# Kernel tuning notes

Measured on AMD Instinct MI355X. Metric: run time of the kernel, lower is better.

The kernel has to match this reference:

```python
import jax, jax.numpy as jnp
from jax import lax
import numpy as np

B, T, D, H, L, O = 64, 256, 256, 256, 50, 2


def setup_inputs() -> dict:
    key = jax.random.key(0)
    ks = jax.random.split(key, 7)
    s = 0.05  # small init to keep gates out of saturation
    return {
        "x": jax.random.normal(ks[0], (B, T, D), jnp.float32),
        "W_ih": jax.random.normal(ks[1], (L, 4 * H, H), jnp.float32) * s,
        "W_hh": jax.random.normal(ks[2], (L, 4 * H, H), jnp.float32) * s,
        "b_ih": jax.random.normal(ks[3], (L, 4 * H), jnp.float32) * s,
        "b_hh": jax.random.normal(ks[4], (L, 4 * H), jnp.float32) * s,
        "W_out": jax.random.normal(ks[5], (O, H), jnp.float32) * s,
        "b_out": jax.random.normal(ks[6], (O,), jnp.float32) * s,
    }


def _lstm_layer(x_seq, wih, whh, bih, bhh):
    # x_seq: [B, T, H_in]; PyTorch gate order i, f, g, o
    b = x_seq.shape[0]
    h = wih.shape[0] // 4
    bias = bih + bhh
    # precompute input projections for all timesteps (one big GEMM)
    xg = jnp.einsum("bti,gi->btg", x_seq, wih) + bias  # [B, T, 4H]

    def step(carry, xg_t):
        hprev, cprev = carry
        gates = xg_t + hprev @ whh.T  # [B, 4H]
        i, f, g, o = jnp.split(gates, 4, axis=-1)
        i = jax.nn.sigmoid(i)
        f = jax.nn.sigmoid(f)
        g = jnp.tanh(g)
        o = jax.nn.sigmoid(o)
        c = f * cprev + i * g
        hnew = o * jnp.tanh(c)
        return (hnew, c), hnew

    h0 = jnp.zeros((b, h), x_seq.dtype)
    (_, _), hs = lax.scan(step, (h0, h0), jnp.swapaxes(xg, 0, 1))
    return jnp.swapaxes(hs, 0, 1)  # [B, T, H]


def reference(x, W_ih, W_hh, b_ih, b_hh, W_out, b_out):
    def layer_step(carry, p):
        wih, whh, bih, bhh = p
        return _lstm_layer(carry, wih, whh, bih, bhh), None

    y, _ = lax.scan(layer_step, x, (W_ih, W_hh, b_ih, b_hh))
    logits = jnp.einsum("bth,oh->bto", y, W_out) + b_out
    return jax.nn.sigmoid(logits)
```

## Files before the change

### kernel.cpp

```cpp
#include <hip/hip_runtime.h>
#include <hip/hip_bf16.h>
#include <stdint.h>
#include <string.h>

#define NB   64
#define NT   256
#define NH   256
#define NL   50
#define NK   512
#define NG   1024

typedef __attribute__((ext_vector_type(8)))  short   short8;
typedef __attribute__((ext_vector_type(8)))  __bf16  bf16x8;
typedef __attribute__((ext_vector_type(4)))  float   float4v;
typedef __attribute__((ext_vector_type(4)))  int     int4v;

__device__ __forceinline__ unsigned short f2bf(float f) {
  union { float f; uint32_t u; } v; v.f = f;
  uint32_t u = v.u;
  uint32_t r = (u + 0x7FFFu + ((u >> 16) & 1u)) >> 16;
  return (unsigned short)r;
}
__device__ __forceinline__ float bf2f(unsigned short s) {
  union { uint32_t u; float f; } v; v.u = ((uint32_t)s) << 16;
  return v.f;
}
__device__ __forceinline__ float sigmoid_f(float x) {
  return 1.0f / (1.0f + __expf(-x));
}
__device__ __forceinline__ float tanh_f(float x) {
  float e = __expf(-2.0f * __builtin_fabsf(x));
  float r = (1.0f - e) / (1.0f + e);
  return __builtin_copysignf(r, x);
}

__device__ __forceinline__ short8 ldg_sc1_b128(const unsigned short* p) {
  short8 r;
  asm volatile("global_load_dwordx4 %0, %1, off sc1" : "=v"(r) : "v"(p) : "memory");
  return r;
}
__device__ __forceinline__ void stg_sc1_b128(unsigned short* p, short8 v) {
  asm volatile("global_store_dwordx4 %0, %1, off sc1" :: "v"(p), "v"(v) : "memory");
}
__device__ __forceinline__ void wait_vm0() {
  asm volatile("s_waitcnt vmcnt(0)" ::: "memory");
}
__device__ __forceinline__ void wave_wait_all4(const int* p) {
  for (;;) {
    int4v f;
    asm volatile("global_load_dwordx4 %0, %1, off sc1\n\ts_waitcnt vmcnt(0)"
                 : "=v"(f) : "v"(p) : "memory");
    if ((f[0] & f[1] & f[2] & f[3]) != 0) break;
  }
}

#define OFF_WSWZ  0
#define OFF_BIAS  52428800
#define OFF_XBF   52633600
#define OFF_HRING 61022208
#define OFF_Y     67575808
#define OFF_PROD  75964416
#define OFF_CONS  76169216

__global__ void prep_w(const float* __restrict__ Wih, const float* __restrict__ Whh,
                       unsigned short* __restrict__ Wswz) {
  int idx = blockIdx.x * 256 + threadIdx.x;
  int j   = idx & 7;
  int lam = (idx >> 3) & 63;
  int kt  = (idx >> 9) & 15;
  int q   = (idx >> 13) & 3;
  int c   = (idx >> 15) & 15;
  int l   = idx >> 19;
  int k   = kt * 32 + (lam >> 4) * 8 + j;
  int g   = q * 256 + c * 16 + (lam & 15);
  float v = (k < 256) ? Wih[(l * NG + g) * 256 + k]
                      : Whh[(l * NG + g) * 256 + (k - 256)];
  Wswz[idx] = f2bf(v);
}

__global__ void prep_bias(const float* __restrict__ bih, const float* __restrict__ bhh,
                          float* __restrict__ Bias) {
  int idx = blockIdx.x * 256 + threadIdx.x;
  int col = idx & 15; int q = (idx >> 4) & 3; int c = (idx >> 6) & 15; int l = idx >> 10;
  int g = q * 256 + c * 16 + col;
  Bias[idx] = bih[l * NG + g] + bhh[l * NG + g];
}

__global__ void prep_x(const float* __restrict__ x, unsigned short* __restrict__ Xbf) {
  int idx = blockIdx.x * 256 + threadIdx.x;
  int d = idx & 255; int t = (idx >> 8) & 255; int b = idx >> 16;
  Xbf[(t * NB + b) * 256 + d] = f2bf(x[idx]);
}

__global__ void zero_flags(int* __restrict__ p) {
  p[blockIdx.x * 256 + threadIdx.x] = 0;
}

#define RSTRIDE 81
#define HSTRIDE 264
__global__ __launch_bounds__(256, 1) void lstm_persistent(
    const unsigned short* __restrict__ Wswz,
    const float* __restrict__ Bias,
    const unsigned short* __restrict__ Xbf,
    unsigned short* __restrict__ Hring,
    unsigned short* __restrict__ Y,
    int* __restrict__ prod4,
    int* __restrict__ cons4) {
  int xcd = blockIdx.x & 7;
  int jj  = blockIdx.x >> 3;
  int l   = xcd * 7 + (jj >> 2);
  int w   = jj & 3;
  if (jj >= 28 || l >= NL) return;
  int tid = threadIdx.x;

  __shared__ unsigned short hc[64 * RSTRIDE * 8];
  __shared__ unsigned short hout[64 * HSTRIDE];

  int wv   = tid >> 6;
  int ln   = tid & 63;
  int c    = w * 4 + wv;
  int colg = ln & 15;
  int quad = ln >> 4;
  bool pvside = (wv & 1);
  int  brb    = wv >> 1;

  bf16x8 wreg[64];
  {
    const unsigned short* wp = Wswz + (size_t)(l * 16 + c) * 32768 + ln * 8;
#pragma unroll
    for (int i = 0; i < 64; ++i)
      wreg[i] = *(const bf16x8*)(wp + i * 512);
  }
  float bv[4];
  {
    const float* bp = Bias + l * NG + c * 64;
#pragma unroll
    for (int q = 0; q < 4; ++q) bv[q] = bp[q * 16 + colg];
  }

  float cr[4][4] = {};
  int j = c * 16 + colg;
  bool last = (l == NL - 1);

  for (int t = 0; t < NT; ++t) {
    {
      short8 v[16];
      int e  = ln & 31;
      int rs = ln >> 5;
      if (!pvside) {
        if (l > 0) wave_wait_all4(&prod4[((l - 1) * NT + t) * 4]);
        const unsigned short* In = (l == 0)
            ? (Xbf + t * (NB * 256))
            : (Hring + (((t & 3) * NL + (l - 1)) * NB) * 256);
#pragma unroll
        for (int i = 0; i < 16; ++i) {
          int b = i * 4 + brb * 2 + rs;
          v[i] = ldg_sc1_b128(In + b * 256 + e * 8);
        }
      } else if (t > 0) {
        wave_wait_all4(&prod4[(l * NT + (t - 1)) * 4]);
        const unsigned short* Pv = Hring + ((((t - 1) & 3) * NL + l) * NB) * 256;
#pragma unroll
        for (int i = 0; i < 16; ++i) {
          int b = i * 4 + brb * 2 + rs;
          v[i] = ldg_sc1_b128(Pv + b * 256 + e * 8);
        }
      } else {
#pragma unroll
        for (int i = 0; i < 16; ++i) v[i] = short8{0, 0, 0, 0, 0, 0, 0, 0};
      }
      wait_vm0();
      int kb = (pvside ? 32 : 0) + e;
#pragma unroll
      for (int i = 0; i < 16; ++i) {
        int b = i * 4 + brb * 2 + rs;
        *(short8*)(hc + (b * RSTRIDE + kb) * 8) = v[i];
      }
    }
    __syncthreads();
    if (tid == 0 && l > 0)
      __hip_atomic_store(&cons4[((l - 1) * NT + t) * 4 + w], 1,
                         __ATOMIC_RELAXED, __HIP_MEMORY_SCOPE_AGENT);

    float4v acc[4][4];
#pragma unroll
    for (int q = 0; q < 4; ++q) {
      float4v f4 = {bv[q], bv[q], bv[q], bv[q]};
#pragma unroll
      for (int m = 0; m < 4; ++m) acc[m][q] = f4;
    }
#pragma unroll
    for (int kt = 0; kt < 16; ++kt) {
      bf16x8 a[4];
#pragma unroll
      for (int m = 0; m < 4; ++m)
        a[m] = *(const bf16x8*)(hc + ((m * 16 + colg) * RSTRIDE + kt * 4 + quad) * 8);
#pragma unroll
      for (int m = 0; m < 4; ++m)
#pragma unroll
        for (int q = 0; q < 4; ++q)
          acc[m][q] = __builtin_amdgcn_mfma_f32_16x16x32_bf16(a[m], wreg[q * 16 + kt], acc[m][q], 0, 0, 0);
    }

#pragma unroll
    for (int m = 0; m < 4; ++m) {
#pragma unroll
      for (int r = 0; r < 4; ++r) {
        int b = m * 16 + quad * 4 + r;
        float gi = sigmoid_f(acc[m][0][r]);
        float gf = sigmoid_f(acc[m][1][r]);
        float gg = tanh_f(acc[m][2][r]);
        float go = sigmoid_f(acc[m][3][r]);
        float cn = gf * cr[m][r] + gi * gg;
        cr[m][r] = cn;
        float h = go * tanh_f(cn);
        hout[b * HSTRIDE + j] = f2bf(h);
      }
    }
    if (wv == 0 && !last && t >= 4) wave_wait_all4(&cons4[(l * NT + (t - 4)) * 4]);
    __syncthreads();

    {
      unsigned short* Hout = Hring + (((t & 3) * NL + l) * NB) * 256;
      unsigned short* Yout = Y + (t * NB) * 256;
#pragma unroll
      for (int pass = 0; pass < 2; ++pass) {
        int u   = pass * 256 + tid;
        int b   = u >> 3;
        int e8  = u & 7;
        int col = w * 64 + e8 * 8;
        short8 hv = *(const short8*)(hout + b * HSTRIDE + col);
        stg_sc1_b128(Hout + b * 256 + col, hv);
        if (last) *(short8*)(Yout + b * 256 + col) = hv;
      }
    }
    __syncthreads();
    if (tid == 0)
      __hip_atomic_store(&prod4[(l * NT + t) * 4 + w], 1,
                         __ATOMIC_RELAXED, __HIP_MEMORY_SCOPE_AGENT);
  }
}

__global__ void final_proj(const unsigned short* __restrict__ Y,
                           const float* __restrict__ Wout,
                           const float* __restrict__ bout,
                           float* __restrict__ out) {
  int t = blockIdx.x;
  int tid = threadIdx.x;
  int b = tid >> 1, o = tid & 1;
  const unsigned short* yrow = Y + (t * NB + b) * 256;
  const float* wr = Wout + o * 256;
  float s = bout[o];
  for (int k0 = 0; k0 < 256; k0 += 8) {
    short8 yv = *(const short8*)(yrow + k0);
#pragma unroll
    for (int e = 0; e < 8; ++e)
      s += bf2f(((unsigned short*)&yv)[e]) * wr[k0 + e];
  }
  out[(b * NT + t) * 2 + o] = 1.0f / (1.0f + __expf(-s));
}

extern "C" void kernel_launch(void* const* d_in, const int* in_sizes, int n_in,
                              void* d_out, int out_size, void* d_ws, size_t ws_size,
                              hipStream_t stream) {
  (void)in_sizes; (void)n_in; (void)out_size; (void)ws_size;
  const float* x    = (const float*)d_in[0];
  const float* Wih  = (const float*)d_in[1];
  const float* Whh  = (const float*)d_in[2];
  const float* bih  = (const float*)d_in[3];
  const float* bhh  = (const float*)d_in[4];
  const float* Wout = (const float*)d_in[5];
  const float* bout = (const float*)d_in[6];
  float* out = (float*)d_out;

  char* ws = (char*)d_ws;
  unsigned short* Wswz  = (unsigned short*)(ws + OFF_WSWZ);
  float*          Bias  = (float*)(ws + OFF_BIAS);
  unsigned short* Xbf   = (unsigned short*)(ws + OFF_XBF);
  unsigned short* Hring = (unsigned short*)(ws + OFF_HRING);
  unsigned short* Y     = (unsigned short*)(ws + OFF_Y);
  int*            prod4 = (int*)(ws + OFF_PROD);
  int*            cons4 = (int*)(ws + OFF_CONS);

  prep_w    <<<102400, 256, 0, stream>>>(Wih, Whh, Wswz);
  prep_bias <<<200,    256, 0, stream>>>(bih, bhh, Bias);
  prep_x    <<<16384,  256, 0, stream>>>(x, Xbf);
  zero_flags<<<400,    256, 0, stream>>>(prod4);

  lstm_persistent<<<256, 256, 0, stream>>>(Wswz, Bias, Xbf, Hring, Y, prod4, cons4);

  final_proj<<<NT, 128, 0, stream>>>(Y, Wout, bout, out);
}
```

Before: 2.434 ms.

## Fold log2e into weights, use exp2/rcp activations, replace trailing barrier with LDS counter

Pre-scales the weights and biases by log2(e), or 2*log2(e) for the g gate, so the gate activations can use raw exp2 and rcp intrinsics with no extra multiplies. tanh is rewritten as 2*sigmoid(2x)-1. The four h values are packed to bf16 with v_cvt_pk_bf16_f32 instead of software rounding. The final __syncthreads is replaced by a per-wave vmcnt wait and an LDS atomic counter, so the last wave to finish publishes the producer flag. This cuts barrier stalls on the serial recurrence path, at the cost of slightly different rounding and reliance on the counter ordering.

```diff
diff --git a/kernel.cpp b/kernel.cpp
--- a/kernel.cpp
+++ b/kernel.cpp
@@ -15,6 +15,9 @@
 typedef __attribute__((ext_vector_type(4)))  float   float4v;
 typedef __attribute__((ext_vector_type(4)))  int     int4v;
 
+#define LOG2E_F    1.44269504088896340736f
+#define TWOLOG2E_F 2.88539008177792681472f
+
 __device__ __forceinline__ unsigned short f2bf(float f) {
   union { float f; uint32_t u; } v; v.f = f;
   uint32_t u = v.u;
@@ -25,13 +28,13 @@
   union { uint32_t u; float f; } v; v.u = ((uint32_t)s) << 16;
   return v.f;
 }
-__device__ __forceinline__ float sigmoid_f(float x) {
-  return 1.0f / (1.0f + __expf(-x));
-}
-__device__ __forceinline__ float tanh_f(float x) {
-  float e = __expf(-2.0f * __builtin_fabsf(x));
-  float r = (1.0f - e) / (1.0f + e);
-  return __builtin_copysignf(r, x);
+__device__ __forceinline__ float sig2(float x) {
+  float e = __builtin_amdgcn_exp2f(-x);
+  return __builtin_amdgcn_rcpf(1.0f + e);
+}
+__device__ __forceinline__ float th2(float x) {
+  float e = __builtin_amdgcn_exp2f(-x);
+  return __builtin_fmaf(2.0f, __builtin_amdgcn_rcpf(1.0f + e), -1.0f);
 }
 
 __device__ __forceinline__ short8 ldg_sc1_b128(const unsigned short* p) {
@@ -75,6 +78,7 @@
   int g   = q * 256 + c * 16 + (lam & 15);
   float v = (k < 256) ? Wih[(l * NG + g) * 256 + k]
                       : Whh[(l * NG + g) * 256 + (k - 256)];
+  v *= (q == 2) ? TWOLOG2E_F : LOG2E_F;
   Wswz[idx] = f2bf(v);
 }
 
@@ -83,7 +87,9 @@
   int idx = blockIdx.x * 256 + threadIdx.x;
   int col = idx & 15; int q = (idx >> 4) & 3; int c = (idx >> 6) & 15; int l = idx >> 10;
   int g = q * 256 + c * 16 + col;
-  Bias[idx] = bih[l * NG + g] + bhh[l * NG + g];
+  float v = bih[l * NG + g] + bhh[l * NG + g];
+  v *= (q == 2) ? TWOLOG2E_F : LOG2E_F;
+  Bias[idx] = v;
 }
 
 __global__ void prep_x(const float* __restrict__ x, unsigned short* __restrict__ Xbf) {
@@ -115,6 +121,7 @@
 
   __shared__ unsigned short hc[64 * RSTRIDE * 8];
   __shared__ unsigned short hout[64 * HSTRIDE];
+  __shared__ int cnt_fl;
 
   int wv   = tid >> 6;
   int ln   = tid & 63;
@@ -123,6 +130,8 @@
   int quad = ln >> 4;
   bool pvside = (wv & 1);
   int  brb    = wv >> 1;
+
+  if (tid == 0) cnt_fl = 0;
 
   bf16x8 wreg[64];
   {
@@ -204,18 +213,25 @@
 
 #pragma unroll
     for (int m = 0; m < 4; ++m) {
+      float hv[4];
 #pragma unroll
       for (int r = 0; r < 4; ++r) {
-        int b = m * 16 + quad * 4 + r;
-        float gi = sigmoid_f(acc[m][0][r]);
-        float gf = sigmoid_f(acc[m][1][r]);
-        float gg = tanh_f(acc[m][2][r]);
-        float go = sigmoid_f(acc[m][3][r]);
+        float gi = sig2(acc[m][0][r]);
+        float gf = sig2(acc[m][1][r]);
+        float gg = th2(acc[m][2][r]);
+        float go = sig2(acc[m][3][r]);
         float cn = gf * cr[m][r] + gi * gg;
         cr[m][r] = cn;
-        float h = go * tanh_f(cn);
-        hout[b * HSTRIDE + j] = f2bf(h);
+        hv[r] = go * th2(cn * TWOLOG2E_F);
       }
+      uint32_t pk01, pk23;
+      asm("v_cvt_pk_bf16_f32 %0, %1, %2" : "=v"(pk01) : "v"(hv[0]), "v"(hv[1]));
+      asm("v_cvt_pk_bf16_f32 %0, %1, %2" : "=v"(pk23) : "v"(hv[2]), "v"(hv[3]));
+      unsigned short* hp = hout + (m * 16 + quad * 4) * HSTRIDE + j;
+      hp[0]           = (unsigned short)pk01;
+      hp[HSTRIDE]     = (unsigned short)(pk01 >> 16);
+      hp[2 * HSTRIDE] = (unsigned short)pk23;
+      hp[3 * HSTRIDE] = (unsigned short)(pk23 >> 16);
     }
     if (wv == 0 && !last && t >= 4) wave_wait_all4(&cons4[(l * NT + (t - 4)) * 4]);
     __syncthreads();
@@ -234,10 +250,13 @@
         if (last) *(short8*)(Yout + b * 256 + col) = hv;
       }
     }
-    __syncthreads();
-    if (tid == 0)
-      __hip_atomic_store(&prod4[(l * NT + t) * 4 + w], 1,
-                         __ATOMIC_RELAXED, __HIP_MEMORY_SCOPE_AGENT);
+    wait_vm0();
+    if (ln == 0) {
+      int old = atomicAdd(&cnt_fl, 1);
+      if (old == 4 * t + 3)
+        __hip_atomic_store(&prod4[(l * NT + t) * 4 + w], 1,
+                           __ATOMIC_RELAXED, __HIP_MEMORY_SCOPE_AGENT);
+    }
   }
 }
 
```

Result: faster. 2.006 ms (-17.6%).
